# Kernel tuning notes

Hardware: AMD Instinct MI355X
Metric: run time of the kernel (lower is better)

Reference implementation:

```python
import jax, jax.numpy as jnp
import numpy as np

EMBED_DIM = 1024
HEAD_SIZE = 64
N_HEAD = 16
N_QUERY_GROUPS = 4
SEQ_LEN = 2048
BATCH = 8


def setup_inputs() -> dict:
    key = jax.random.key(0)
    ks = jax.random.split(key, 7)
    s = 1.0 / np.sqrt(EMBED_DIM)
    x = jax.random.normal(ks[0], (BATCH, SEQ_LEN, EMBED_DIM), dtype=jnp.float32)
    Wq = jax.random.uniform(ks[1], (EMBED_DIM, N_HEAD * HEAD_SIZE), jnp.float32, -s, s)
    bq = jax.random.uniform(ks[2], (N_HEAD * HEAD_SIZE,), jnp.float32, -s, s)
    Wk = jax.random.uniform(ks[3], (EMBED_DIM, N_QUERY_GROUPS * HEAD_SIZE), jnp.float32, -s, s)
    bk = jax.random.uniform(ks[4], (N_QUERY_GROUPS * HEAD_SIZE,), jnp.float32, -s, s)
    Wv = jax.random.uniform(ks[5], (EMBED_DIM, N_QUERY_GROUPS * HEAD_SIZE), jnp.float32, -s, s)
    bv = jax.random.uniform(ks[6], (N_QUERY_GROUPS * HEAD_SIZE,), jnp.float32, -s, s)
    return {"x": x, "Wq": Wq, "bq": bq, "Wk": Wk, "bk": bk, "Wv": Wv, "bv": bv}


def reference(x, Wq, bq, Wk, bk, Wv, bv):
    B, T, _ = x.shape
    rep = N_HEAD // N_QUERY_GROUPS  # queries per group
    Q = x @ Wq + bq  # (B, T, H*hs)
    # GQA: torch .repeat tiles the group-block [g0..g3, g0..g3, ...]
    K = (x @ Wk + bk).reshape(B, T, N_QUERY_GROUPS, HEAD_SIZE)
    K = jnp.tile(K, (1, 1, rep, 1)).reshape(B, T, N_HEAD * HEAD_SIZE)
    V = (x @ Wv + bv).reshape(B, T, N_QUERY_GROUPS, HEAD_SIZE)
    V = jnp.tile(V, (1, 1, rep, 1)).reshape(B, T, N_HEAD * HEAD_SIZE)
    # flattened-head scores: contract over full H*hs dim (as in source)
    att = jnp.einsum('btd,bsd->bts', Q, K)  # (B, T, T)
    causal = jnp.triu(jnp.ones((T, T), dtype=bool), k=1)
    mask = jnp.where(causal, jnp.float32(-jnp.inf), jnp.float32(0.0))[None, None]  # (1,1,T,T)
    att = att + mask  # broadcasts to (1, B, T, T), matching torch semantics
    att = jax.nn.softmax(att, axis=-1) / jnp.sqrt(jnp.float32(HEAD_SIZE))  # post-hoc scale, as in source
    out = jnp.einsum('xbts,bsd->xbtd', att, V)  # (1, B, T, H*hs)
    return out
```

## Files before the change

kernel.cpp:

```cpp
#include <hip/hip_runtime.h>
#include <float.h>
#include <stdint.h>

#define T_ 2048
#define DG 256

typedef _Float16 half8 __attribute__((ext_vector_type(8)));
typedef _Float16 half4v __attribute__((ext_vector_type(4)));
typedef __fp16 fp16x2 __attribute__((ext_vector_type(2)));
typedef float f32x4 __attribute__((ext_vector_type(4)));
typedef float f32x16 __attribute__((ext_vector_type(16)));
typedef unsigned uint2v __attribute__((ext_vector_type(2)));

__device__ __forceinline__ void gload16(const void* g, void* l) {
  __builtin_amdgcn_global_load_lds(
      (const __attribute__((address_space(1))) unsigned int*)g,
      (__attribute__((address_space(3))) unsigned int*)l, 16, 0, 0);
}
#define WAIT_VMC(N)  do { asm volatile("s_waitcnt vmcnt(" #N ")" ::: "memory"); __builtin_amdgcn_sched_barrier(0); } while (0)
#define WAIT_LGKM0() do { asm volatile("s_waitcnt lgkmcnt(0)" ::: "memory"); __builtin_amdgcn_sched_barrier(0); } while (0)

__device__ __forceinline__ float cross32(float x, int g) {
  unsigned u = __builtin_bit_cast(unsigned, x);
  uint2v r = __builtin_amdgcn_permlane32_swap(u, u, false, false);
  return __builtin_bit_cast(float, g ? r[0] : r[1]);
}

__global__ __launch_bounds__(256) void prep_w(
    const float* __restrict__ Wq, const float* __restrict__ bq,
    const float* __restrict__ Wk, const float* __restrict__ bk,
    const float* __restrict__ Wv, const float* __restrict__ bv,
    _Float16* __restrict__ Wt, float* __restrict__ bcat) {
  int idx = blockIdx.x * 256 + threadIdx.x;
  int n = idx >> 10, k = idx & 1023;
  float v;
  if (n < 256)      v = Wq[k * 1024 + n] + Wq[k * 1024 + n + 256]
                      + Wq[k * 1024 + n + 512] + Wq[k * 1024 + n + 768];
  else if (n < 512) v = Wk[k * 256 + n - 256];
  else              v = Wv[k * 256 + n - 512];
  Wt[idx] = (_Float16)v;
  if (k == 0) {
    float bb;
    if (n < 256)      bb = bq[n] + bq[n + 256] + bq[n + 512] + bq[n + 768];
    else if (n < 512) bb = bk[n - 256];
    else              bb = bv[n - 512];
    bcat[n] = bb;
  }
}

__global__ __launch_bounds__(256) void qkv_gemm(
    const float* __restrict__ x, const _Float16* __restrict__ Wt,
    const float* __restrict__ bcat,
    _Float16* __restrict__ Qh, _Float16* __restrict__ Kh, _Float16* __restrict__ Vt) {
  __shared__ __align__(16) uint8_t smem[49152];
  const int tid = threadIdx.x;
  const int w = tid >> 6, l = tid & 63;
  const int wr = w >> 1, wc = w & 1;
  const int lr = l & 15, lk = l >> 4;
  const int m0 = blockIdx.x * 128, n0 = blockIdx.y * 128;

  f32x4 acc[4][4] = {};

  auto stage = [&](int k0, int buf) {
    uint8_t* Ab = smem + buf * 24576;
    uint8_t* Bb = Ab + 16384;
#pragma unroll
    for (int i = 0; i < 4; ++i) {
      int si = i * 256 + tid;
      int row = si >> 3, p = si & 7;
      gload16(x + (size_t)(m0 + row) * 1024 + k0 + ((p ^ (row & 7)) << 2), Ab + si * 16);
    }
#pragma unroll
    for (int i = 0; i < 2; ++i) {
      int si = i * 256 + tid;
      int row = si >> 2, p = si & 3;
      gload16(Wt + (size_t)(n0 + row) * 1024 + k0 + ((p ^ (row & 3)) << 3), Bb + si * 16);
    }
  };

  stage(0, 0);
  __syncthreads();

  for (int kt = 0; kt < 32; ++kt) {
    int cur = kt & 1;
    if (kt < 31) stage((kt + 1) * 32, cur ^ 1);
    const uint8_t* Ab = smem + cur * 24576;
    const uint8_t* Bb = Ab + 16384;
    half8 af[4], bf[4];
#pragma unroll
    for (int mi = 0; mi < 4; ++mi) {
      int row = wr * 64 + mi * 16 + lr;
      const float* pa = (const float*)(Ab + row * 128);
      f32x4 a0 = *(const f32x4*)(pa + ((((lk << 1))     ^ (row & 7)) << 2));
      f32x4 a1 = *(const f32x4*)(pa + ((((lk << 1) | 1) ^ (row & 7)) << 2));
      half8 h;
#pragma unroll
      for (int j = 0; j < 4; ++j) { h[j] = (_Float16)a0[j]; h[j + 4] = (_Float16)a1[j]; }
      af[mi] = h;
    }
#pragma unroll
    for (int ni = 0; ni < 4; ++ni) {
      int row = wc * 64 + ni * 16 + lr;
      bf[ni] = *(const half8*)(Bb + row * 64 + ((lk ^ (row & 3)) << 4));
    }
#pragma unroll
    for (int mi = 0; mi < 4; ++mi)
#pragma unroll
      for (int ni = 0; ni < 4; ++ni)
        acc[mi][ni] = __builtin_amdgcn_mfma_f32_16x16x32_f16(af[mi], bf[ni], acc[mi][ni], 0, 0, 0);
    __syncthreads();
  }

#pragma unroll
  for (int mi = 0; mi < 4; ++mi) {
#pragma unroll
    for (int ni = 0; ni < 4; ++ni) {
      int ng = n0 + wc * 64 + ni * 16 + lr;
      int mg = m0 + wr * 64 + mi * 16 + lk * 4;
      float bias = bcat[ng];
      if (ng < 256) {
#pragma unroll
        for (int r = 0; r < 4; ++r)
          Qh[(size_t)(mg + r) * DG + ng] = (_Float16)((acc[mi][ni][r] + bias) * 1.44269504f);
      } else if (ng < 512) {
#pragma unroll
        for (int r = 0; r < 4; ++r)
          Kh[(size_t)(mg + r) * DG + (ng - 256)] = (_Float16)(acc[mi][ni][r] + bias);
      } else {
        half4v h;
#pragma unroll
        for (int r = 0; r < 4; ++r) h[r] = (_Float16)(acc[mi][ni][r] + bias);
        *(half4v*)(Vt + ((size_t)((mg >> 11) * DG + (ng - 512))) * T_ + (mg & 2047)) = h;
      }
    }
  }
}

__global__ __launch_bounds__(128, 1) void attn_mfma(
    const _Float16* __restrict__ Qg, const _Float16* __restrict__ Kg,
    const _Float16* __restrict__ Vtg, float* __restrict__ out) {
  __shared__ __align__(16) uint8_t smem[65536];
  const int tid = threadIdx.x;
  const int wv = tid >> 6;
  const int l  = tid & 63;
  const int g  = l >> 5;
  const int ln = l & 31;
  const int bid = blockIdx.x;
  const int b   = bid & 7;
  const int tile = (bid < 256) ? (63 - (bid >> 3)) : ((bid - 256) >> 3);
  const int q0 = tile * 32;

  const _Float16* Kb = Kg  + (size_t)b * T_ * DG;
  const _Float16* Vb = Vtg + (size_t)b * DG * T_;

  const _Float16* Qrow = Qg + ((size_t)(b * T_ + q0 + ln)) * DG + 8 * g;
  half8 qf[16];
#pragma unroll
  for (int kk = 0; kk < 16; ++kk) qf[kk] = *(const half8*)(Qrow + kk * 16);

  f32x16 o[8] = {};
  float m_r = -1e30f, l_r = 0.0f;

  uint8_t* myK = smem + wv * 32768;
  auto stageK = [&](int s0, int buf) {
    uint8_t* Kl = myK + buf * 16384;
#pragma unroll
    for (int i = 0; i < 16; ++i) {
      int slot = i * 64 + l;
      int row = slot >> 5, part = slot & 31;
      gload16(Kb + (size_t)(s0 + row) * DG + ((part ^ (row & 7)) << 3), Kl + i * 1024);
    }
  };

  int cur = 0;
  if (wv <= tile) stageK(wv * 32, 0);

  for (int kt = wv; kt <= tile; kt += 2) {
    if (kt + 2 <= tile) { stageK((kt + 2) * 32, cur ^ 1); WAIT_VMC(16); }
    else                { WAIT_VMC(0); }
    int s0 = kt * 32;
    uint8_t* Klds = myK + cur * 16384;

    f32x16 sa = {}, sb = {};
    const int xr = (ln & 7) << 4;
    __builtin_amdgcn_s_setprio(1);
#pragma unroll
    for (int kk = 0; kk < 16; kk += 2) {
      half8 ka = *(const half8*)(Klds + ln * 512 + ((kk * 32 + 16 * g) ^ xr));
      half8 kb = *(const half8*)(Klds + ln * 512 + (((kk + 1) * 32 + 16 * g) ^ xr));
      sa = __builtin_amdgcn_mfma_f32_32x32x16_f16(ka, qf[kk],     sa, 0, 0, 0);
      sb = __builtin_amdgcn_mfma_f32_32x32x16_f16(kb, qf[kk + 1], sb, 0, 0, 0);
    }
    __builtin_amdgcn_s_setprio(0);

    half8 vf0[8], vf1[8];
#pragma unroll
    for (int dt = 0; dt < 8; ++dt) {
      const _Float16* vr = Vb + (size_t)(dt * 32 + ln) * T_ + s0 + 8 * g;
      vf0[dt] = *(const half8*)vr;
      vf1[dt] = *(const half8*)(vr + 16);
    }

    float s[16];
#pragma unroll
    for (int r = 0; r < 16; ++r) s[r] = sa[r] + sb[r];
    if (kt == tile) {
#pragma unroll
      for (int r = 0; r < 16; ++r) {
        int srow = (r & 3) + 8 * (r >> 2) + 4 * g;
        if (srow > ln) s[r] = -1e30f;
      }
    }
    float pmax = s[0];
#pragma unroll
    for (int r = 1; r < 16; ++r) pmax = fmaxf(pmax, s[r]);
    pmax = fmaxf(pmax, cross32(pmax, g));
    if (!__all(pmax <= m_r + 8.0f)) {
      float mnew = fmaxf(m_r, pmax);
      float sc = __builtin_amdgcn_exp2f(m_r - mnew);
      l_r *= sc;
#pragma unroll
      for (int dt = 0; dt < 8; ++dt)
#pragma unroll
        for (int r = 0; r < 16; ++r) o[dt][r] *= sc;
      m_r = mnew;
    }
    float p[16]; float psum = 0.0f;
#pragma unroll
    for (int r = 0; r < 16; ++r) { p[r] = __builtin_amdgcn_exp2f(s[r] - m_r); psum += p[r]; }
    l_r += psum + cross32(psum, g);

    unsigned ph[8];
#pragma unroll
    for (int i = 0; i < 8; ++i) {
      fp16x2 t2 = __builtin_amdgcn_cvt_pkrtz(p[2 * i], p[2 * i + 1]);
      ph[i] = __builtin_bit_cast(unsigned, t2);
    }
    union U { unsigned u[4]; half8 h; };
    U f0, f1;
    {
      uint2v r02 = __builtin_amdgcn_permlane32_swap(ph[0], ph[2], false, false);
      uint2v r13 = __builtin_amdgcn_permlane32_swap(ph[1], ph[3], false, false);
      uint2v r46 = __builtin_amdgcn_permlane32_swap(ph[4], ph[6], false, false);
      uint2v r57 = __builtin_amdgcn_permlane32_swap(ph[5], ph[7], false, false);
      f0.u[0] = r02[0]; f0.u[2] = r02[1];
      f0.u[1] = r13[0]; f0.u[3] = r13[1];
      f1.u[0] = r46[0]; f1.u[2] = r46[1];
      f1.u[1] = r57[0]; f1.u[3] = r57[1];
    }

    __builtin_amdgcn_s_setprio(1);
#pragma unroll
    for (int dt = 0; dt < 8; ++dt)
      o[dt] = __builtin_amdgcn_mfma_f32_32x32x16_f16(vf0[dt], f0.h, o[dt], 0, 0, 0);
#pragma unroll
    for (int dt = 0; dt < 8; ++dt)
      o[dt] = __builtin_amdgcn_mfma_f32_32x32x16_f16(vf1[dt], f1.h, o[dt], 0, 0, 0);
    __builtin_amdgcn_s_setprio(0);
    cur ^= 1;
  }

  __syncthreads();
  if (wv == 1) {
    float* dst = (float*)(smem + 32768);
#pragma unroll
    for (int dt = 0; dt < 8; ++dt)
#pragma unroll
      for (int r = 0; r < 16; ++r)
        dst[(dt * 16 + r) * 64 + l] = o[dt][r];
    ((float*)smem)[l]      = m_r;
    ((float*)smem)[64 + l] = l_r;
  }
  __syncthreads();
  if (wv == 0) {
    float m1 = ((float*)smem)[l];
    float l1 = ((float*)smem)[64 + l];
    float M   = fmaxf(m_r, m1);
    float sc0 = __builtin_amdgcn_exp2f(m_r - M);
    float sc1 = __builtin_amdgcn_exp2f(m1 - M);
    float lt  = l_r * sc0 + l1 * sc1;
    float inv = 1.0f / (lt * 8.0f);
    const float* src = (const float*)(smem + 32768);
    float* chunk = (float*)(smem + 4096);
    float* ob = out + ((size_t)(b * T_ + q0)) * 1024;
#pragma unroll
    for (int dt = 0; dt < 8; ++dt) {
      WAIT_LGKM0();
#pragma unroll
      for (int r = 0; r < 16; ++r) {
        int dl = (r & 3) + 8 * (r >> 2) + 4 * g;
        float merged = (o[dt][r] * sc0 + src[(dt * 16 + r) * 64 + l] * sc1) * inv;
        chunk[ln * 33 + dl] = merged;
      }
      WAIT_LGKM0();
#pragma unroll
      for (int rr = 0; rr < 2; ++rr) {
        int qq = (l >> 2) + 16 * rr;
        int cp = (l & 3) * 8;
        float vv[8];
#pragma unroll
        for (int jj = 0; jj < 8; ++jj) vv[jj] = chunk[qq * 33 + cp + jj];
        float4 w0 = make_float4(vv[0], vv[1], vv[2], vv[3]);
        float4 w1 = make_float4(vv[4], vv[5], vv[6], vv[7]);
        float* orow = ob + (size_t)qq * 1024 + dt * 32 + cp;
#pragma unroll
        for (int rep = 0; rep < 4; ++rep) {
          *(float4*)(orow + rep * 256)     = w0;
          *(float4*)(orow + rep * 256 + 4) = w1;
        }
      }
    }
  }
}

extern "C" void kernel_launch(void* const* d_in, const int* in_sizes, int n_in,
                              void* d_out, int out_size, void* d_ws, size_t ws_size,
                              hipStream_t stream) {
  const float* x  = (const float*)d_in[0];
  const float* Wq = (const float*)d_in[1];
  const float* bq = (const float*)d_in[2];
  const float* Wk = (const float*)d_in[3];
  const float* bk = (const float*)d_in[4];
  const float* Wv = (const float*)d_in[5];
  const float* bv = (const float*)d_in[6];
  float* out = (float*)d_out;
  char* ws = (char*)d_ws;
  _Float16* Wt   = (_Float16*)ws;
  float*    bcat = (float*)(ws + 0x180000);
  _Float16* Qh   = (_Float16*)(ws + 0x181000);
  _Float16* Kh   = Qh + (size_t)16384 * 256;
  _Float16* Vt   = Kh + (size_t)16384 * 256;

  prep_w<<<3072, 256, 0, stream>>>(Wq, bq, Wk, bk, Wv, bv, Wt, bcat);
  qkv_gemm<<<dim3(128, 6), 256, 0, stream>>>(x, Wt, bcat, Qh, Kh, Vt);
  attn_mfma<<<512, 128, 0, stream>>>(Qh, Kh, Vt, out);
}
```

Baseline: 136.5 us.

## Split attention across four waves, load K directly, widen QKV GEMM tile

The attention kernel now runs four waves per block instead of two, and each wave takes every fourth key tile. K tiles are read straight from global memory into registers instead of being staged in LDS with async loads. The cross-wave softmax merge becomes a two-level tree reduction through shared memory. The QKV GEMM tile widens to 128x256, so each blockIdx.y maps to exactly one of Q, K or V. That cuts the grid and lets each block reuse its x loads across more columns, at the cost of more accumulator registers and lower occupancy.

```diff
diff --git a/kernel.cpp b/kernel.cpp
--- a/kernel.cpp
+++ b/kernel.cpp
@@ -17,7 +17,6 @@
       (const __attribute__((address_space(1))) unsigned int*)g,
       (__attribute__((address_space(3))) unsigned int*)l, 16, 0, 0);
 }
-#define WAIT_VMC(N)  do { asm volatile("s_waitcnt vmcnt(" #N ")" ::: "memory"); __builtin_amdgcn_sched_barrier(0); } while (0)
 #define WAIT_LGKM0() do { asm volatile("s_waitcnt lgkmcnt(0)" ::: "memory"); __builtin_amdgcn_sched_barrier(0); } while (0)
 
 __device__ __forceinline__ float cross32(float x, int g) {
@@ -52,17 +51,19 @@
     const float* __restrict__ x, const _Float16* __restrict__ Wt,
     const float* __restrict__ bcat,
     _Float16* __restrict__ Qh, _Float16* __restrict__ Kh, _Float16* __restrict__ Vt) {
-  __shared__ __align__(16) uint8_t smem[49152];
+  __shared__ __align__(16) uint8_t smem[65536];
   const int tid = threadIdx.x;
   const int w = tid >> 6, l = tid & 63;
   const int wr = w >> 1, wc = w & 1;
   const int lr = l & 15, lk = l >> 4;
-  const int m0 = blockIdx.x * 128, n0 = blockIdx.y * 128;
-
-  f32x4 acc[4][4] = {};
+  const int m0 = blockIdx.x * 128;
+  const int by = blockIdx.y;
+  const int n0 = by * 256;
+
+  f32x4 acc[4][8] = {};
 
   auto stage = [&](int k0, int buf) {
-    uint8_t* Ab = smem + buf * 24576;
+    uint8_t* Ab = smem + buf * 32768;
     uint8_t* Bb = Ab + 16384;
 #pragma unroll
     for (int i = 0; i < 4; ++i) {
@@ -71,7 +72,7 @@
       gload16(x + (size_t)(m0 + row) * 1024 + k0 + ((p ^ (row & 7)) << 2), Ab + si * 16);
     }
 #pragma unroll
-    for (int i = 0; i < 2; ++i) {
+    for (int i = 0; i < 4; ++i) {
       int si = i * 256 + tid;
       int row = si >> 2, p = si & 3;
       gload16(Wt + (size_t)(n0 + row) * 1024 + k0 + ((p ^ (row & 3)) << 3), Bb + si * 16);
@@ -84,9 +85,9 @@
   for (int kt = 0; kt < 32; ++kt) {
     int cur = kt & 1;
     if (kt < 31) stage((kt + 1) * 32, cur ^ 1);
-    const uint8_t* Ab = smem + cur * 24576;
+    const uint8_t* Ab = smem + cur * 32768;
     const uint8_t* Bb = Ab + 16384;
-    half8 af[4], bf[4];
+    half8 af[4], bf[8];
 #pragma unroll
     for (int mi = 0; mi < 4; ++mi) {
       int row = wr * 64 + mi * 16 + lr;
@@ -99,14 +100,14 @@
       af[mi] = h;
     }
 #pragma unroll
-    for (int ni = 0; ni < 4; ++ni) {
-      int row = wc * 64 + ni * 16 + lr;
+    for (int ni = 0; ni < 8; ++ni) {
+      int row = wc * 128 + ni * 16 + lr;
       bf[ni] = *(const half8*)(Bb + row * 64 + ((lk ^ (row & 3)) << 4));
     }
 #pragma unroll
     for (int mi = 0; mi < 4; ++mi)
 #pragma unroll
-      for (int ni = 0; ni < 4; ++ni)
+      for (int ni = 0; ni < 8; ++ni)
         acc[mi][ni] = __builtin_amdgcn_mfma_f32_16x16x32_f16(af[mi], bf[ni], acc[mi][ni], 0, 0, 0);
     __syncthreads();
   }
@@ -114,32 +115,32 @@
 #pragma unroll
   for (int mi = 0; mi < 4; ++mi) {
 #pragma unroll
-    for (int ni = 0; ni < 4; ++ni) {
-      int ng = n0 + wc * 64 + ni * 16 + lr;
+    for (int ni = 0; ni < 8; ++ni) {
+      int nl = wc * 128 + ni * 16 + lr;
       int mg = m0 + wr * 64 + mi * 16 + lk * 4;
-      float bias = bcat[ng];
-      if (ng < 256) {
+      float bias = bcat[n0 + nl];
+      if (by == 0) {
 #pragma unroll
         for (int r = 0; r < 4; ++r)
-          Qh[(size_t)(mg + r) * DG + ng] = (_Float16)((acc[mi][ni][r] + bias) * 1.44269504f);
-      } else if (ng < 512) {
+          Qh[(size_t)(mg + r) * DG + nl] = (_Float16)((acc[mi][ni][r] + bias) * 1.44269504f);
+      } else if (by == 1) {
 #pragma unroll
         for (int r = 0; r < 4; ++r)
-          Kh[(size_t)(mg + r) * DG + (ng - 256)] = (_Float16)(acc[mi][ni][r] + bias);
+          Kh[(size_t)(mg + r) * DG + nl] = (_Float16)(acc[mi][ni][r] + bias);
       } else {
         half4v h;
 #pragma unroll
         for (int r = 0; r < 4; ++r) h[r] = (_Float16)(acc[mi][ni][r] + bias);
-        *(half4v*)(Vt + ((size_t)((mg >> 11) * DG + (ng - 512))) * T_ + (mg & 2047)) = h;
+        *(half4v*)(Vt + ((size_t)((mg >> 11) * DG + nl)) * T_ + (mg & 2047)) = h;
       }
     }
   }
 }
 
-__global__ __launch_bounds__(128, 1) void attn_mfma(
+__global__ __launch_bounds__(256) void attn_mfma(
     const _Float16* __restrict__ Qg, const _Float16* __restrict__ Kg,
     const _Float16* __restrict__ Vtg, float* __restrict__ out) {
-  __shared__ __align__(16) uint8_t smem[65536];
+  __shared__ __align__(16) uint8_t smem[67584];
   const int tid = threadIdx.x;
   const int wv = tid >> 6;
   const int l  = tid & 63;
@@ -161,35 +162,19 @@
   f32x16 o[8] = {};
   float m_r = -1e30f, l_r = 0.0f;
 
-  uint8_t* myK = smem + wv * 32768;
-  auto stageK = [&](int s0, int buf) {
-    uint8_t* Kl = myK + buf * 16384;
-#pragma unroll
-    for (int i = 0; i < 16; ++i) {
-      int slot = i * 64 + l;
-      int row = slot >> 5, part = slot & 31;
-      gload16(Kb + (size_t)(s0 + row) * DG + ((part ^ (row & 7)) << 3), Kl + i * 1024);
-    }
-  };
-
-  int cur = 0;
-  if (wv <= tile) stageK(wv * 32, 0);
-
-  for (int kt = wv; kt <= tile; kt += 2) {
-    if (kt + 2 <= tile) { stageK((kt + 2) * 32, cur ^ 1); WAIT_VMC(16); }
-    else                { WAIT_VMC(0); }
+  for (int kt = wv; kt <= tile; kt += 4) {
     int s0 = kt * 32;
-    uint8_t* Klds = myK + cur * 16384;
+    const _Float16* krow = Kb + (size_t)(s0 + ln) * DG + 8 * g;
+    half8 kf[16];
+#pragma unroll
+    for (int kk = 0; kk < 16; ++kk) kf[kk] = *(const half8*)(krow + kk * 16);
 
     f32x16 sa = {}, sb = {};
-    const int xr = (ln & 7) << 4;
     __builtin_amdgcn_s_setprio(1);
 #pragma unroll
     for (int kk = 0; kk < 16; kk += 2) {
-      half8 ka = *(const half8*)(Klds + ln * 512 + ((kk * 32 + 16 * g) ^ xr));
-      half8 kb = *(const half8*)(Klds + ln * 512 + (((kk + 1) * 32 + 16 * g) ^ xr));
-      sa = __builtin_amdgcn_mfma_f32_32x32x16_f16(ka, qf[kk],     sa, 0, 0, 0);
-      sb = __builtin_amdgcn_mfma_f32_32x32x16_f16(kb, qf[kk + 1], sb, 0, 0, 0);
+      sa = __builtin_amdgcn_mfma_f32_32x32x16_f16(kf[kk],     qf[kk],     sa, 0, 0, 0);
+      sb = __builtin_amdgcn_mfma_f32_32x32x16_f16(kf[kk + 1], qf[kk + 1], sb, 0, 0, 0);
     }
     __builtin_amdgcn_s_setprio(0);
 
@@ -257,31 +242,58 @@
     for (int dt = 0; dt < 8; ++dt)
       o[dt] = __builtin_amdgcn_mfma_f32_32x32x16_f16(vf1[dt], f1.h, o[dt], 0, 0, 0);
     __builtin_amdgcn_s_setprio(0);
-    cur ^= 1;
-  }
-
-  __syncthreads();
-  if (wv == 1) {
-    float* dst = (float*)(smem + 32768);
+  }
+
+  float* ml = (float*)(smem + 65536);
+  __syncthreads();
+  if (wv & 1) {
+    float* dst = (float*)(smem + (wv >> 1) * 32768);
 #pragma unroll
     for (int dt = 0; dt < 8; ++dt)
 #pragma unroll
       for (int r = 0; r < 16; ++r)
         dst[(dt * 16 + r) * 64 + l] = o[dt][r];
-    ((float*)smem)[l]      = m_r;
-    ((float*)smem)[64 + l] = l_r;
+    ml[wv * 128 + l]      = m_r;
+    ml[wv * 128 + 64 + l] = l_r;
+  }
+  __syncthreads();
+  if (!(wv & 1)) {
+    float m1 = ml[(wv + 1) * 128 + l];
+    float l1 = ml[(wv + 1) * 128 + 64 + l];
+    float M   = fmaxf(m_r, m1);
+    float sc0 = __builtin_amdgcn_exp2f(m_r - M);
+    float sc1 = __builtin_amdgcn_exp2f(m1 - M);
+    const float* src = (const float*)(smem + (wv >> 1) * 32768);
+#pragma unroll
+    for (int dt = 0; dt < 8; ++dt)
+#pragma unroll
+      for (int r = 0; r < 16; ++r)
+        o[dt][r] = o[dt][r] * sc0 + src[(dt * 16 + r) * 64 + l] * sc1;
+    l_r = l_r * sc0 + l1 * sc1;
+    m_r = M;
+  }
+  __syncthreads();
+  if (wv == 2) {
+    float* dst = (float*)(smem + 32768);
+#pragma unroll
+    for (int dt = 0; dt < 8; ++dt)
+#pragma unroll
+      for (int r = 0; r < 16; ++r)
+        dst[(dt * 16 + r) * 64 + l] = o[dt][r];
+    ml[2 * 128 + l]      = m_r;
+    ml[2 * 128 + 64 + l] = l_r;
   }
   __syncthreads();
   if (wv == 0) {
-    float m1 = ((float*)smem)[l];
-    float l1 = ((float*)smem)[64 + l];
+    float m1 = ml[2 * 128 + l];
+    float l1 = ml[2 * 128 + 64 + l];
     float M   = fmaxf(m_r, m1);
     float sc0 = __builtin_amdgcn_exp2f(m_r - M);
     float sc1 = __builtin_amdgcn_exp2f(m1 - M);
     float lt  = l_r * sc0 + l1 * sc1;
     float inv = 1.0f / (lt * 8.0f);
     const float* src = (const float*)(smem + 32768);
-    float* chunk = (float*)(smem + 4096);
+    float* chunk = (float*)smem;
     float* ob = out + ((size_t)(b * T_ + q0)) * 1024;
 #pragma unroll
     for (int dt = 0; dt < 8; ++dt) {
@@ -332,6 +344,6 @@
   _Float16* Vt   = Kh + (size_t)16384 * 256;
 
   prep_w<<<3072, 256, 0, stream>>>(Wq, bq, Wk, bk, Wv, bv, Wt, bcat);
-  qkv_gemm<<<dim3(128, 6), 256, 0, stream>>>(x, Wt, bcat, Qh, Kh, Vt);
-  attn_mfma<<<512, 128, 0, stream>>>(Qh, Kh, Vt, out);
-}
+  qkv_gemm<<<dim3(128, 3), 256, 0, stream>>>(x, Wt, bcat, Qh, Kh, Vt);
+  attn_mfma<<<512, 256, 0, stream>>>(Qh, Kh, Vt, out);
+}
```

Measured after the change: 177.6 us. +30.1%, slower.
